# Kernel optimization log

Hardware: AMD Instinct MI355X
Metric: run time of the kernel (lower is better)

Reference implementation:

```python
import jax, jax.numpy as jnp
import numpy as np

N_NODES = 50000
HEADS1 = 4
NEG_SLOPE = 0.2
EPS = 1e-16


def gat_conv(x, edge_index, W, att_src, att_dst, bias, heads, out_ch, concat):
    # edge_index: [2, E] with self-loops already appended by caller
    src, dst = edge_index[0], edge_index[1]
    N = x.shape[0]
    h = (x @ W).reshape(N, heads, out_ch)                      # [N, H, C]
    a_src = jnp.sum(h * att_src, axis=-1)                      # [N, H]
    a_dst = jnp.sum(h * att_dst, axis=-1)                      # [N, H]
    e = a_src[src] + a_dst[dst]                                # [E, H]
    e = jnp.where(e > 0, e, NEG_SLOPE * e)                     # leaky_relu
    m = jax.ops.segment_max(e, dst, num_segments=N)            # [N, H]
    alpha = jnp.exp(e - m[dst])                                # [E, H]
    denom = jax.ops.segment_sum(alpha, dst, num_segments=N)    # [N, H]
    alpha = alpha / (denom[dst] + EPS)                         # [E, H]
    msg = alpha[:, :, None] * h[src]                           # [E, H, C]
    out = jax.ops.segment_sum(msg, dst, num_segments=N)        # [N, H, C]
    if concat:
        out = out.reshape(N, heads * out_ch)
    else:
        out = out.mean(axis=1)
    return out + bias, alpha


def setup_inputs() -> dict:
    key = jax.random.key(0)
    ks = jax.random.split(key, 12)
    N, F, H, heads, C, E = N_NODES, 256, 64, HEADS1, 40, 800000
    g = 0.1
    return {
        "x": jax.random.normal(ks[0], (N, F), dtype=jnp.float32),
        "edge_index": jax.random.randint(ks[1], (2, E), 0, N, dtype=jnp.int32),
        "W1": jax.random.normal(ks[2], (F, heads * H), dtype=jnp.float32) * g,
        "att_src1": jax.random.normal(ks[3], (heads, H), dtype=jnp.float32) * g,
        "att_dst1": jax.random.normal(ks[4], (heads, H), dtype=jnp.float32) * g,
        "b1": jnp.zeros((heads * H,), dtype=jnp.float32),
        "W2": jax.random.normal(ks[5], (heads * H, C), dtype=jnp.float32) * g,
        "att_src2": jax.random.normal(ks[6], (1, C), dtype=jnp.float32) * g,
        "att_dst2": jax.random.normal(ks[7], (1, C), dtype=jnp.float32) * g,
        "b2": jnp.zeros((C,), dtype=jnp.float32),
    }


def reference(x, edge_index, W1, att_src1, att_dst1, b1, W2, att_src2, att_dst2, b2):
    N = x.shape[0]
    # add self-loops (PyG GATConv default)
    loops = jnp.arange(N, dtype=edge_index.dtype)
    ei = jnp.concatenate([edge_index, jnp.stack([loops, loops])], axis=1)
    # dropout is identity in eval mode
    h1, alpha = gat_conv(x, ei, W1, att_src1, att_dst1, b1,
                         HEADS1, W1.shape[1] // HEADS1, concat=True)
    h1 = jax.nn.elu(h1)
    h2, _ = gat_conv(h1, ei, W2, att_src2, att_dst2, b2,
                     1, W2.shape[1], concat=False)
    return jax.nn.log_softmax(h2, axis=1), alpha
```

## Files before the change

kernel.cpp:

```cpp
#include <hip/hip_runtime.h>
#include <math.h>

#define N_NODES 50000
#define HC1 256
#define H1 4
#define C2 40
#define C2P 64
#define E0 800000
#define ET 850000
#define NEG_SLOPE 0.2f
#define EPS_A 1e-16f

typedef __bf16 bf16x8 __attribute__((ext_vector_type(8)));
typedef float f32x4 __attribute__((ext_vector_type(4)));
typedef unsigned short u16x8 __attribute__((ext_vector_type(8)));


__device__ inline unsigned short f2bf(float f) {
    unsigned u = __float_as_uint(f);
    return (unsigned short)((u + 0x7FFFu + ((u >> 16) & 1u)) >> 16);
}
__device__ inline float bf_lo(unsigned q) { return __uint_as_float(q << 16); }
__device__ inline float bf_hi(unsigned q) { return __uint_as_float(q & 0xFFFF0000u); }


__device__ inline int edge_src(const int* __restrict__ ei, int e) {
    return (e < E0) ? ei[e] : (e - E0);
}
__device__ inline int edge_dst(const int* __restrict__ ei, int e) {
    return (e < E0) ? ei[E0 + e] : (e - E0);
}

__device__ inline void acc8(float ac[8], float A, uint4 q) {
    ac[0] += A * bf_lo(q.x); ac[1] += A * bf_hi(q.x);
    ac[2] += A * bf_lo(q.y); ac[3] += A * bf_hi(q.y);
    ac[4] += A * bf_lo(q.z); ac[5] += A * bf_hi(q.z);
    ac[6] += A * bf_lo(q.w); ac[7] += A * bf_hi(q.w);
}

__device__ inline float leaky(float v) { return v > 0.f ? v : NEG_SLOPE * v; }


#define CV_X 3200000
#define CV_W1 65536
#define CV_W2 16384
#define CV_TOT (CV_X + CV_W1 + CV_W2 + N_NODES)

__global__ void convert_all_kernel(const float* __restrict__ x,
                                   const float* __restrict__ W1,
                                   const float* __restrict__ W2,
                                   ushort4* __restrict__ xbf,
                                   unsigned short* __restrict__ w1t,
                                   unsigned short* __restrict__ w2t,
                                   int* __restrict__ deg) {
    int tid = blockIdx.x * blockDim.x + threadIdx.x;
    if (tid < CV_X) {
        float4 v = ((const float4*)x)[tid];
        ushort4 w;
        w.x = f2bf(v.x); w.y = f2bf(v.y); w.z = f2bf(v.z); w.w = f2bf(v.w);
        xbf[tid] = w;
    } else if (tid < CV_X + CV_W1) {
        int i = tid - CV_X;
        int n = i >> 8, k = i & 255;
        w1t[i] = f2bf(W1[k * 256 + n]);
    } else if (tid < CV_X + CV_W1 + CV_W2) {
        int i = tid - CV_X - CV_W1;
        int n = i >> 8, k = i & 255;
        w2t[i] = (n < C2) ? f2bf(W2[k * C2 + n]) : (unsigned short)0;
    } else if (tid < CV_TOT) {
        deg[tid - CV_X - CV_W1 - CV_W2] = 0;
    }
}


__global__ void hist_kernel(const int* __restrict__ ei, int* __restrict__ deg) {
    int e = blockIdx.x * blockDim.x + threadIdx.x;
    if (e >= ET) return;
    atomicAdd(&deg[edge_dst(ei, e)], 1);
}

__global__ __launch_bounds__(256) void scan_block_kernel(const int* __restrict__ deg,
                                                         int* __restrict__ excl,
                                                         int* __restrict__ bsum) {
    __shared__ int tmp[256];
    int t = threadIdx.x;
    int i = blockIdx.x * 256 + t;
    int v = (i < N_NODES) ? deg[i] : 0;
    tmp[t] = v;
    __syncthreads();
#pragma unroll
    for (int o = 1; o < 256; o <<= 1) {
        int x = (t >= o) ? tmp[t - o] : 0;
        __syncthreads();
        tmp[t] += x;
        __syncthreads();
    }
    if (i < N_NODES) excl[i] = tmp[t] - v;
    if (t == 255) bsum[blockIdx.x] = tmp[255];
}

#define NSCAN_B 196

__global__ __launch_bounds__(256) void scan_top_kernel(int* __restrict__ bsum) {
    __shared__ int tmp[256];
    int t = threadIdx.x;
    int v = (t < NSCAN_B) ? bsum[t] : 0;
    tmp[t] = v;
    __syncthreads();
#pragma unroll
    for (int o = 1; o < 256; o <<= 1) {
        int x = (t >= o) ? tmp[t - o] : 0;
        __syncthreads();
        tmp[t] += x;
        __syncthreads();
    }
    if (t < NSCAN_B) bsum[t] = tmp[t] - v;
}

__global__ __launch_bounds__(256) void scan_add_kernel(int* __restrict__ offsets,
                                                       int* __restrict__ cursor,
                                                       const int* __restrict__ bsum) {
    int i = blockIdx.x * 256 + threadIdx.x;
    if (i < N_NODES) {
        int v = offsets[i] + bsum[blockIdx.x];
        offsets[i] = v;
        cursor[i] = v;
    }
    if (i == 0) offsets[N_NODES] = ET;
}

__global__ void scatter_kernel(const int* __restrict__ ei, int* __restrict__ cursor,
                               int2* __restrict__ csr_es) {
    int e = blockIdx.x * blockDim.x + threadIdx.x;
    if (e >= ET) return;
    int d = edge_dst(ei, e);
    int pos = atomicAdd(&cursor[d], 1);
    csr_es[pos] = make_int2(e, edge_src(ei, e));
}


template <int TBM, int TBN, int WROWS, int WCOLS>
__global__ __launch_bounds__(256) void gemm_mfma_kernel(const unsigned short* __restrict__ Abf,
                                                        const unsigned short* __restrict__ Bt,
                                                        unsigned short* __restrict__ Cbf,
                                                        const float* __restrict__ att_s,
                                                        const float* __restrict__ att_d,
                                                        float* __restrict__ a_src_o,
                                                        float* __restrict__ a_dst_o,
                                                        int M, int Nc, int attN, int hstride) {
    static_assert(TBM == WROWS * 64 && TBN == WCOLS * 64, "tile");
    constexpr int LDK = 40;
    __shared__ alignas(16) unsigned short As[TBM * LDK];
    __shared__ alignas(16) unsigned short Bs[TBN * LDK];
    const int t = threadIdx.x;
    const int lane = t & 63;
    const int w = t >> 6;
    const int quad = lane >> 4;
    const int l16 = lane & 15;
    const int wm = (w / WCOLS) * 64;
    const int wn = (w % WCOLS) * 64;
    const int bm = blockIdx.x * TBM;
    const int bn = blockIdx.y * TBN;

    f32x4 acc[4][4] = {};

    for (int k0 = 0; k0 < 256; k0 += 32) {
        __syncthreads();
#pragma unroll
        for (int i = 0; i < TBM / 64; ++i) {
            int idx = t + i * 256;
            int row = idx >> 2, seg = idx & 3;
            u16x8 v = {};
            if (bm + row < M)
                v = *(const u16x8*)(Abf + (size_t)(bm + row) * 256 + k0 + seg * 8);
            *(u16x8*)&As[row * LDK + seg * 8] = v;
        }
#pragma unroll
        for (int i = 0; i < TBN / 64; ++i) {
            int idx = t + i * 256;
            int row = idx >> 2, seg = idx & 3;
            u16x8 v = *(const u16x8*)(Bt + (size_t)(bn + row) * 256 + k0 + seg * 8);
            *(u16x8*)&Bs[row * LDK + seg * 8] = v;
        }
        __syncthreads();

        bf16x8 af[4], bfr[4];
#pragma unroll
        for (int mi = 0; mi < 4; ++mi)
            af[mi] = *(const bf16x8*)&As[(wm + mi * 16 + l16) * LDK + quad * 8];
#pragma unroll
        for (int ni = 0; ni < 4; ++ni)
            bfr[ni] = *(const bf16x8*)&Bs[(wn + ni * 16 + l16) * LDK + quad * 8];
#pragma unroll
        for (int mi = 0; mi < 4; ++mi)
#pragma unroll
            for (int ni = 0; ni < 4; ++ni)
                acc[mi][ni] = __builtin_amdgcn_mfma_f32_16x16x32_bf16(
                    af[mi], bfr[ni], acc[mi][ni], 0, 0, 0);
    }

#pragma unroll
    for (int mi = 0; mi < 4; ++mi)
#pragma unroll
        for (int ni = 0; ni < 4; ++ni)
#pragma unroll
            for (int r = 0; r < 4; ++r) {
                int row = bm + wm + mi * 16 + quad * 4 + r;
                int col = bn + wn + ni * 16 + l16;
                if (row < M)
                    Cbf[(size_t)row * Nc + col] = f2bf(acc[mi][ni][r]);
            }

    float asc[4], adc[4];
#pragma unroll
    for (int ni = 0; ni < 4; ++ni) {
        int col = bn + wn + ni * 16 + l16;
        bool valid = col < attN;
        asc[ni] = valid ? att_s[col] : 0.f;
        adc[ni] = valid ? att_d[col] : 0.f;
    }
    float vs[16], vd[16];
#pragma unroll
    for (int mi = 0; mi < 4; ++mi)
#pragma unroll
        for (int r = 0; r < 4; ++r) {
            float s = 0.f, dd = 0.f;
#pragma unroll
            for (int ni = 0; ni < 4; ++ni) {
                s += acc[mi][ni][r] * asc[ni];
                dd += acc[mi][ni][r] * adc[ni];
            }
            vs[mi * 4 + r] = s;
            vd[mi * 4 + r] = dd;
        }
#pragma unroll
    for (int k = 0; k < 4; ++k) {
        const int o = 1 << k;
        const int b = (l16 >> k) & 1;
#pragma unroll
        for (int j = 0; j < (8 >> k); ++j) {
            float lo = vs[2 * j], hi = vs[2 * j + 1];
            float keep = b ? hi : lo, send = b ? lo : hi;
            vs[j] = keep + __shfl_xor(send, o);
            lo = vd[2 * j]; hi = vd[2 * j + 1];
            keep = b ? hi : lo; send = b ? lo : hi;
            vd[j] = keep + __shfl_xor(send, o);
        }
    }
    {
        int mi = l16 >> 2, r = l16 & 3;
        int row = bm + wm + mi * 16 + quad * 4 + r;
        int head = (bn + wn) >> 6;
        if (row < M) {
            a_src_o[(size_t)row * hstride + head] = vs[0];
            a_dst_o[(size_t)row * hstride + head] = vd[0];
        }
    }
}


#define L1_LOADQ(q, jb)                                                         \
    _Pragma("unroll")                                                           \
    for (int k = 0; k < 4; ++k) {                                               \
        int s_ = __shfl(esy, shbase + (jb) + k);                                \
        q[k] = *(const uint4*)&h1bf[(unsigned)s_ * 128u + 4u * li];             \
    }

#define L1_FMAQ(q, jb)                                                          \
    _Pragma("unroll")                                                           \
    for (int k = 0; k < 4; ++k) {                                               \
        float A_ = aw[4 * ((jb) + k) + headc];                                  \
        acc8(ac, A_, q[k]);                                                     \
    }

__global__ __launch_bounds__(256) void l1_fused_kernel(const int* __restrict__ off,
                                                       const int2* __restrict__ csr_es,
                                                       const float4* __restrict__ a_src4,
                                                       const float4* __restrict__ a_dst4,
                                                       const unsigned* __restrict__ h1bf,
                                                       const float* __restrict__ b1,
                                                       float4* __restrict__ alpha_out4,
                                                       unsigned* __restrict__ out1bf) {
    __shared__ int    s_w[4][2][32];
    __shared__ float4 p_w[4][2][32];
    int t = threadIdx.x;
    int w = t >> 6, lane = t & 63;
    int half = lane >> 5, li = lane & 31;
    int shbase = half << 5;
    int d = blockIdx.x * 8 + w * 2 + half;
    int beg = off[d], end = off[d + 1];
    int deg = end - beg;
    int nch = (deg + 31) >> 5;
    int cnt0 = min(deg, 32);
    bool act0 = li < cnt0;
    float4 ad4 = a_dst4[d];
    int headc = li >> 3;

    float ac[8] = {};
    float4 sum = make_float4(0.f, 0.f, 0.f, 0.f);
    float4 mx = make_float4(-INFINITY, -INFINITY, -INFINITY, -INFINITY);
    int2 es0 = make_int2(0, 0);
    float4 p0 = make_float4(0.f, 0.f, 0.f, 0.f);

    const float* aw = (const float*)&p_w[w][half][0];
    const int*   sw = &s_w[w][half][0];

    if (nch == 1) {
        float4 l0 = make_float4(-INFINITY, -INFINITY, -INFINITY, -INFINITY);
        float4 as4 = make_float4(0.f, 0.f, 0.f, 0.f);
        if (act0) {
            es0 = csr_es[beg + li];
            as4 = a_src4[es0.y];
        }
        int esy = es0.y;
        const int B = (cnt0 + 3) >> 2;

        uint4 qa[4], qb[4];
        L1_LOADQ(qa, 0);
        if (B > 1) { L1_LOADQ(qb, 4); }

        if (act0) {
            l0.x = leaky(as4.x + ad4.x);
            l0.y = leaky(as4.y + ad4.y);
            l0.z = leaky(as4.z + ad4.z);
            l0.w = leaky(as4.w + ad4.w);
        }
        mx = l0;
#pragma unroll
        for (int o = 1; o <= 16; o <<= 1) {
            mx.x = fmaxf(mx.x, __shfl_xor(mx.x, o));
            mx.y = fmaxf(mx.y, __shfl_xor(mx.y, o));
            mx.z = fmaxf(mx.z, __shfl_xor(mx.z, o));
            mx.w = fmaxf(mx.w, __shfl_xor(mx.w, o));
        }
        p0.x = __expf(l0.x - mx.x);
        p0.y = __expf(l0.y - mx.y);
        p0.z = __expf(l0.z - mx.z);
        p0.w = __expf(l0.w - mx.w);
        p_w[w][half][li] = p0;
        sum = p0;

        int i = 0;
        for (; i + 2 <= B; i += 2) {
            L1_FMAQ(qa, i * 4);
            if (i + 2 < B) { L1_LOADQ(qa, (i + 2) * 4); }
            L1_FMAQ(qb, i * 4 + 4);
            if (i + 3 < B) { L1_LOADQ(qb, (i + 3) * 4); }
        }
        if (i < B) { L1_FMAQ(qa, i * 4); }
    } else {
        for (int cc = 0; cc < nch; ++cc) {
            int idx = beg + cc * 32 + li;
            if (idx < end) {
                int2 es = csr_es[idx];
                float4 as4 = a_src4[es.y];
                mx.x = fmaxf(mx.x, leaky(as4.x + ad4.x));
                mx.y = fmaxf(mx.y, leaky(as4.y + ad4.y));
                mx.z = fmaxf(mx.z, leaky(as4.z + ad4.z));
                mx.w = fmaxf(mx.w, leaky(as4.w + ad4.w));
            }
        }
#pragma unroll
        for (int o = 1; o <= 16; o <<= 1) {
            mx.x = fmaxf(mx.x, __shfl_xor(mx.x, o));
            mx.y = fmaxf(mx.y, __shfl_xor(mx.y, o));
            mx.z = fmaxf(mx.z, __shfl_xor(mx.z, o));
            mx.w = fmaxf(mx.w, __shfl_xor(mx.w, o));
        }
        for (int cc = 0; cc < nch; ++cc) {
            int idx = beg + cc * 32 + li;
            if (idx < end) {
                int2 es = csr_es[idx];
                float4 as4 = a_src4[es.y];
                sum.x += __expf(leaky(as4.x + ad4.x) - mx.x);
                sum.y += __expf(leaky(as4.y + ad4.y) - mx.y);
                sum.z += __expf(leaky(as4.z + ad4.z) - mx.z);
                sum.w += __expf(leaky(as4.w + ad4.w) - mx.w);
            }
        }
    }

#pragma unroll
    for (int o = 1; o <= 16; o <<= 1) {
        sum.x += __shfl_xor(sum.x, o);
        sum.y += __shfl_xor(sum.y, o);
        sum.z += __shfl_xor(sum.z, o);
        sum.w += __shfl_xor(sum.w, o);
    }
    float4 inv;
    inv.x = 1.f / (sum.x + EPS_A); inv.y = 1.f / (sum.y + EPS_A);
    inv.z = 1.f / (sum.z + EPS_A); inv.w = 1.f / (sum.w + EPS_A);
    float invh = (headc == 0) ? inv.x : (headc == 1) ? inv.y
               : (headc == 2) ? inv.z : inv.w;

    if (nch == 1) {
        if (act0) {
            float4 al0;
            al0.x = p0.x * inv.x; al0.y = p0.y * inv.y;
            al0.z = p0.z * inv.z; al0.w = p0.w * inv.w;
            alpha_out4[es0.x] = al0;
        }
    } else {
        for (int cc = 0; cc < nch; ++cc) {
            int idx = beg + cc * 32 + li;
            int cnt = min(32, deg - cc * 32);
            if (idx < end) {
                int2 es = csr_es[idx];
                float4 as4 = a_src4[es.y];
                float4 p;
                p.x = __expf(leaky(as4.x + ad4.x) - mx.x);
                p.y = __expf(leaky(as4.y + ad4.y) - mx.y);
                p.z = __expf(leaky(as4.z + ad4.z) - mx.z);
                p.w = __expf(leaky(as4.w + ad4.w) - mx.w);
                float4 al;
                al.x = p.x * inv.x; al.y = p.y * inv.y;
                al.z = p.z * inv.z; al.w = p.w * inv.w;
                alpha_out4[es.x] = al;
                s_w[w][half][li] = es.y;
                p_w[w][half][li] = p;
            }
            for (int j = 0; j < cnt; ++j) {
                int s = sw[j];
                float A = aw[4 * j + headc];
                uint4 q = *(const uint4*)&h1bf[(unsigned)s * 128u + 4u * li];
                acc8(ac, A, q);
            }
        }
    }

#pragma unroll
    for (int c = 0; c < 8; ++c) ac[c] *= invh;

    float4 bb0 = *(const float4*)&b1[8 * li];
    float4 bb1 = *(const float4*)&b1[8 * li + 4];
    float v0 = ac[0] + bb0.x, v1 = ac[1] + bb0.y;
    float v2 = ac[2] + bb0.z, v3 = ac[3] + bb0.w;
    float v4 = ac[4] + bb1.x, v5 = ac[5] + bb1.y;
    float v6 = ac[6] + bb1.z, v7 = ac[7] + bb1.w;
    v0 = v0 > 0.f ? v0 : __expf(v0) - 1.f;
    v1 = v1 > 0.f ? v1 : __expf(v1) - 1.f;
    v2 = v2 > 0.f ? v2 : __expf(v2) - 1.f;
    v3 = v3 > 0.f ? v3 : __expf(v3) - 1.f;
    v4 = v4 > 0.f ? v4 : __expf(v4) - 1.f;
    v5 = v5 > 0.f ? v5 : __expf(v5) - 1.f;
    v6 = v6 > 0.f ? v6 : __expf(v6) - 1.f;
    v7 = v7 > 0.f ? v7 : __expf(v7) - 1.f;
    uint4 qo;
    qo.x = ((unsigned)f2bf(v1) << 16) | (unsigned)f2bf(v0);
    qo.y = ((unsigned)f2bf(v3) << 16) | (unsigned)f2bf(v2);
    qo.z = ((unsigned)f2bf(v5) << 16) | (unsigned)f2bf(v4);
    qo.w = ((unsigned)f2bf(v7) << 16) | (unsigned)f2bf(v6);
    *(uint4*)&out1bf[(size_t)d * 128 + 4 * li] = qo;
}


#define L2_LOADQ(q, jb)                                                         \
    _Pragma("unroll")                                                           \
    for (int k = 0; k < 4; ++k) {                                               \
        int s_ = __shfl(s0, shbase + (jb) + k);                                 \
        q[k] = h2bf[(unsigned)s_ * 32u + li];                                   \
    }

#define L2_FMAQ(q, jb)                                                          \
    _Pragma("unroll")                                                           \
    for (int k = 0; k < 4; ++k) {                                               \
        float A_ = __shfl(p0, shbase + (jb) + k);                               \
        acc0 += A_ * bf_lo(q[k]);                                               \
        acc1 += A_ * bf_hi(q[k]);                                               \
    }

__global__ __launch_bounds__(256) void l2_fused_kernel(const int* __restrict__ off,
                                                       const int2* __restrict__ csr_es,
                                                       const float* __restrict__ a_src,
                                                       const float* __restrict__ a_dst,
                                                       const unsigned* __restrict__ h2bf,
                                                       const float* __restrict__ b2,
                                                       float* __restrict__ out) {
    __shared__ uint2 sp_w[4][2][32];
    int t = threadIdx.x;
    int w = t >> 6, lane = t & 63;
    int half = lane >> 5, li = lane & 31;
    int shbase = half << 5;
    int d = blockIdx.x * 8 + w * 2 + half;
    int beg = off[d], end = off[d + 1];
    int deg = end - beg;
    float ad = a_dst[d];
    int nch = (deg + 31) >> 5;
    int cnt0 = min(deg, 32);
    bool act0 = li < cnt0;

    float sum = 0.f, acc0 = 0.f, acc1 = 0.f;
    float p0 = 0.f;

    if (nch == 1) {
        float el0 = -INFINITY; int s0 = 0;
        if (act0) {
            int2 es = csr_es[beg + li];
            s0 = es.y;
            el0 = leaky(a_src[s0] + ad);
        }
        const int B = (cnt0 + 3) >> 2;
        unsigned qa[4], qb[4];
        L2_LOADQ(qa, 0);
        if (B > 1) { L2_LOADQ(qb, 4); }

        float mx = el0;
#pragma unroll
        for (int o = 1; o <= 16; o <<= 1) mx = fmaxf(mx, __shfl_xor(mx, o));
        p0 = __expf(el0 - mx);
        sum = p0;

        int i = 0;
        for (; i + 2 <= B; i += 2) {
            L2_FMAQ(qa, i * 4);
            if (i + 2 < B) { L2_LOADQ(qa, (i + 2) * 4); }
            L2_FMAQ(qb, i * 4 + 4);
            if (i + 3 < B) { L2_LOADQ(qb, (i + 3) * 4); }
        }
        if (i < B) { L2_FMAQ(qa, i * 4); }
    } else {
        float mx = -INFINITY;
        for (int cc = 0; cc < nch; ++cc) {
            int idx = beg + cc * 32 + li;
            if (idx < end) {
                int2 es = csr_es[idx];
                mx = fmaxf(mx, leaky(a_src[es.y] + ad));
            }
        }
#pragma unroll
        for (int o = 1; o <= 16; o <<= 1) mx = fmaxf(mx, __shfl_xor(mx, o));
        for (int cc = 0; cc < nch; ++cc) {
            int idx = beg + cc * 32 + li;
            int cnt = min(32, deg - cc * 32);
            if (idx < end) {
                int2 es = csr_es[idx];
                float el = leaky(a_src[es.y] + ad);
                float p = __expf(el - mx);
                sum += p;
                sp_w[w][half][li] = make_uint2((unsigned)es.y, __float_as_uint(p));
            }
            for (int j = 0; j < cnt; ++j) {
                uint2 e0 = sp_w[w][half][j];
                float A0 = __uint_as_float(e0.y);
                unsigned q = h2bf[e0.x * 32u + li];
                acc0 += A0 * bf_lo(q);
                acc1 += A0 * bf_hi(q);
            }
        }
    }

#pragma unroll
    for (int o = 1; o <= 16; o <<= 1) sum += __shfl_xor(sum, o);
    float inv = 1.f / (sum + EPS_A);
    acc0 *= inv;
    acc1 *= inv;

    bool act = li < 20;
    float v0 = act ? acc0 + b2[2 * li]     : -INFINITY;
    float v1 = act ? acc1 + b2[2 * li + 1] : -INFINITY;
    float mmx = fmaxf(v0, v1);
#pragma unroll
    for (int o = 16; o; o >>= 1) mmx = fmaxf(mmx, __shfl_xor(mmx, o));
    float ex = act ? __expf(v0 - mmx) + __expf(v1 - mmx) : 0.f;
#pragma unroll
    for (int o = 16; o; o >>= 1) ex += __shfl_xor(ex, o);
    float ls = __logf(ex);
    if (act)
        *(float2*)&out[(size_t)d * C2 + 2 * li] = make_float2(v0 - mmx - ls, v1 - mmx - ls);
}


extern "C" void kernel_launch(void* const* d_in, const int* in_sizes, int n_in,
                              void* d_out, int out_size, void* d_ws, size_t ws_size,
                              hipStream_t stream) {
    const float* x   = (const float*)d_in[0];
    const int*   ei  = (const int*)d_in[1];
    const float* W1  = (const float*)d_in[2];
    const float* as1 = (const float*)d_in[3];
    const float* ad1 = (const float*)d_in[4];
    const float* b1  = (const float*)d_in[5];
    const float* W2  = (const float*)d_in[6];
    const float* as2 = (const float*)d_in[7];
    const float* ad2 = (const float*)d_in[8];
    const float* b2  = (const float*)d_in[9];

    float* out   = (float*)d_out;
    float* alpha = out + (size_t)N_NODES * C2;

    unsigned* u32    = (unsigned*)d_ws;
    unsigned* h1bf   = u32;
    unsigned* xbf    = h1bf + 6400000;
    unsigned* h2bf   = xbf + 6400000;
    unsigned* w1t    = h2bf + 1600000;
    unsigned* w2t    = w1t + 32768;
    float* a_src1    = (float*)(w2t + 8192);
    float* a_dst1    = a_src1 + 200000;
    float* a_src2    = a_dst1 + 200000;
    float* a_dst2    = a_src2 + 50000;
    int*   deg       = (int*)(a_dst2 + 50000);
    int*   offs      = deg + 50000;
    int*   cursor    = offs + 50001;
    int*   bsum      = cursor + 50000;
    int2*  csr_es    = (int2*)(bsum + 257);
    unsigned* out1bf = xbf;

    const int TB = 256;
    const int EB = (ET + TB - 1) / TB;

    convert_all_kernel<<<(CV_TOT + TB - 1) / TB, TB, 0, stream>>>(
        x, W1, W2, (ushort4*)xbf, (unsigned short*)w1t, (unsigned short*)w2t, deg);

    hist_kernel<<<EB, TB, 0, stream>>>(ei, deg);
    scan_block_kernel<<<NSCAN_B, TB, 0, stream>>>(deg, offs, bsum);
    scan_top_kernel<<<1, TB, 0, stream>>>(bsum);
    scan_add_kernel<<<NSCAN_B, TB, 0, stream>>>(offs, cursor, bsum);
    scatter_kernel<<<EB, TB, 0, stream>>>(ei, cursor, csr_es);

    gemm_mfma_kernel<128, 128, 2, 2><<<dim3((N_NODES + 127) / 128, 2), TB, 0, stream>>>(
        (const unsigned short*)xbf, (const unsigned short*)w1t, (unsigned short*)h1bf,
        as1, ad1, a_src1, a_dst1, N_NODES, HC1, 256, H1);
    l1_fused_kernel<<<N_NODES / 8, TB, 0, stream>>>(offs, csr_es,
                                                    (const float4*)a_src1,
                                                    (const float4*)a_dst1,
                                                    h1bf, b1, (float4*)alpha, out1bf);

    gemm_mfma_kernel<256, 64, 4, 1><<<dim3((N_NODES + 255) / 256, 1), TB, 0, stream>>>(
        (const unsigned short*)out1bf, (const unsigned short*)w2t, (unsigned short*)h2bf,
        as2, ad2, a_src2, a_dst2, N_NODES, C2P, C2, 1);
    l2_fused_kernel<<<N_NODES / 8, TB, 0, stream>>>(offs, csr_es, a_src2, a_dst2,
                                                    h2bf, b2, out);
}
```

Baseline: 358.9 us.

## Fuse degree histogram into convert, double-buffer GEMM LDS, batch layer-2 gathers

The degree histogram moves into the conversion kernel, with the deg array zeroed by a memset, which removes one kernel launch. The bf16 GEMM now double-buffers its shared-memory tiles and prefetches the next k-slice before the current MFMAs, dropping one barrier per iteration. The layer-2 single-chunk path issues up to eight gather loads up front instead of a two-deep rotation, which raises memory-level parallelism at the cost of more registers. There is a possible race: the prefetch writes buffer cur^1 after only one barrier, so other waves may still be reading that buffer from the previous iteration.

```diff
diff --git a/kernel.cpp b/kernel.cpp
--- a/kernel.cpp
+++ b/kernel.cpp
@@ -44,11 +44,12 @@
 #define CV_X 3200000
 #define CV_W1 65536
 #define CV_W2 16384
-#define CV_TOT (CV_X + CV_W1 + CV_W2 + N_NODES)
+#define CV_TOT (CV_X + CV_W1 + CV_W2 + ET)
 
 __global__ void convert_all_kernel(const float* __restrict__ x,
                                    const float* __restrict__ W1,
                                    const float* __restrict__ W2,
+                                   const int* __restrict__ ei,
                                    ushort4* __restrict__ xbf,
                                    unsigned short* __restrict__ w1t,
                                    unsigned short* __restrict__ w2t,
@@ -68,16 +69,11 @@
         int n = i >> 8, k = i & 255;
         w2t[i] = (n < C2) ? f2bf(W2[k * C2 + n]) : (unsigned short)0;
     } else if (tid < CV_TOT) {
-        deg[tid - CV_X - CV_W1 - CV_W2] = 0;
-    }
-}
-
-
-__global__ void hist_kernel(const int* __restrict__ ei, int* __restrict__ deg) {
-    int e = blockIdx.x * blockDim.x + threadIdx.x;
-    if (e >= ET) return;
-    atomicAdd(&deg[edge_dst(ei, e)], 1);
-}
+        int e = tid - CV_X - CV_W1 - CV_W2;
+        atomicAdd(&deg[edge_dst(ei, e)], 1);
+    }
+}
+
 
 __global__ __launch_bounds__(256) void scan_block_kernel(const int* __restrict__ deg,
                                                          int* __restrict__ excl,
@@ -138,6 +134,24 @@
     csr_es[pos] = make_int2(e, edge_src(ei, e));
 }
 
+
+#define GEMM_STAGE(k0v, bufv)                                                     \
+    _Pragma("unroll")                                                             \
+    for (int i = 0; i < TBM / 64; ++i) {                                          \
+        int idx = t + i * 256;                                                    \
+        int row = idx >> 2, seg = idx & 3;                                        \
+        u16x8 v = {};                                                             \
+        if (bm + row < M)                                                         \
+            v = *(const u16x8*)(Abf + (size_t)(bm + row) * 256 + (k0v) + seg * 8);\
+        *(u16x8*)&As[bufv][row * LDK + seg * 8] = v;                              \
+    }                                                                             \
+    _Pragma("unroll")                                                             \
+    for (int i = 0; i < TBN / 64; ++i) {                                          \
+        int idx = t + i * 256;                                                    \
+        int row = idx >> 2, seg = idx & 3;                                        \
+        u16x8 v = *(const u16x8*)(Bt + (size_t)(bn + row) * 256 + (k0v) + seg * 8);\
+        *(u16x8*)&Bs[bufv][row * LDK + seg * 8] = v;                              \
+    }
 
 template <int TBM, int TBN, int WROWS, int WCOLS>
 __global__ __launch_bounds__(256) void gemm_mfma_kernel(const unsigned short* __restrict__ Abf,
@@ -150,8 +164,8 @@
                                                         int M, int Nc, int attN, int hstride) {
     static_assert(TBM == WROWS * 64 && TBN == WCOLS * 64, "tile");
     constexpr int LDK = 40;
-    __shared__ alignas(16) unsigned short As[TBM * LDK];
-    __shared__ alignas(16) unsigned short Bs[TBN * LDK];
+    __shared__ alignas(16) unsigned short As[2][TBM * LDK];
+    __shared__ alignas(16) unsigned short Bs[2][TBN * LDK];
     const int t = threadIdx.x;
     const int lane = t & 63;
     const int w = t >> 6;
@@ -164,39 +178,26 @@
 
     f32x4 acc[4][4] = {};
 
+    GEMM_STAGE(0, 0);
+    int cur = 0;
     for (int k0 = 0; k0 < 256; k0 += 32) {
         __syncthreads();
-#pragma unroll
-        for (int i = 0; i < TBM / 64; ++i) {
-            int idx = t + i * 256;
-            int row = idx >> 2, seg = idx & 3;
-            u16x8 v = {};
-            if (bm + row < M)
-                v = *(const u16x8*)(Abf + (size_t)(bm + row) * 256 + k0 + seg * 8);
-            *(u16x8*)&As[row * LDK + seg * 8] = v;
-        }
-#pragma unroll
-        for (int i = 0; i < TBN / 64; ++i) {
-            int idx = t + i * 256;
-            int row = idx >> 2, seg = idx & 3;
-            u16x8 v = *(const u16x8*)(Bt + (size_t)(bn + row) * 256 + k0 + seg * 8);
-            *(u16x8*)&Bs[row * LDK + seg * 8] = v;
-        }
-        __syncthreads();
+        if (k0 + 32 < 256) { GEMM_STAGE(k0 + 32, cur ^ 1); }
 
         bf16x8 af[4], bfr[4];
 #pragma unroll
         for (int mi = 0; mi < 4; ++mi)
-            af[mi] = *(const bf16x8*)&As[(wm + mi * 16 + l16) * LDK + quad * 8];
+            af[mi] = *(const bf16x8*)&As[cur][(wm + mi * 16 + l16) * LDK + quad * 8];
 #pragma unroll
         for (int ni = 0; ni < 4; ++ni)
-            bfr[ni] = *(const bf16x8*)&Bs[(wn + ni * 16 + l16) * LDK + quad * 8];
+            bfr[ni] = *(const bf16x8*)&Bs[cur][(wn + ni * 16 + l16) * LDK + quad * 8];
 #pragma unroll
         for (int mi = 0; mi < 4; ++mi)
 #pragma unroll
             for (int ni = 0; ni < 4; ++ni)
                 acc[mi][ni] = __builtin_amdgcn_mfma_f32_16x16x32_bf16(
                     af[mi], bfr[ni], acc[mi][ni], 0, 0, 0);
+        cur ^= 1;
     }
 
 #pragma unroll
@@ -500,9 +501,10 @@
             el0 = leaky(a_src[s0] + ad);
         }
         const int B = (cnt0 + 3) >> 2;
-        unsigned qa[4], qb[4];
-        L2_LOADQ(qa, 0);
-        if (B > 1) { L2_LOADQ(qb, 4); }
+        unsigned q[8][4];
+#pragma unroll
+        for (int i = 0; i < 8; ++i)
+            if (i < B) { L2_LOADQ(q[i], i * 4); }
 
         float mx = el0;
 #pragma unroll
@@ -510,14 +512,9 @@
         p0 = __expf(el0 - mx);
         sum = p0;
 
-        int i = 0;
-        for (; i + 2 <= B; i += 2) {
-            L2_FMAQ(qa, i * 4);
-            if (i + 2 < B) { L2_LOADQ(qa, (i + 2) * 4); }
-            L2_FMAQ(qb, i * 4 + 4);
-            if (i + 3 < B) { L2_LOADQ(qb, (i + 3) * 4); }
-        }
-        if (i < B) { L2_FMAQ(qa, i * 4); }
+#pragma unroll
+        for (int i = 0; i < 8; ++i)
+            if (i < B) { L2_FMAQ(q[i], i * 4); }
     } else {
         float mx = -INFINITY;
         for (int cc = 0; cc < nch; ++cc) {
@@ -542,9 +539,9 @@
             for (int j = 0; j < cnt; ++j) {
                 uint2 e0 = sp_w[w][half][j];
                 float A0 = __uint_as_float(e0.y);
-                unsigned q = h2bf[e0.x * 32u + li];
-                acc0 += A0 * bf_lo(q);
-                acc1 += A0 * bf_hi(q);
+                unsigned qv = h2bf[e0.x * 32u + li];
+                acc0 += A0 * bf_lo(qv);
+                acc1 += A0 * bf_hi(qv);
             }
         }
     }
@@ -607,10 +604,11 @@
     const int TB = 256;
     const int EB = (ET + TB - 1) / TB;
 
+    hipMemsetAsync(deg, 0, (size_t)N_NODES * sizeof(int), stream);
+
     convert_all_kernel<<<(CV_TOT + TB - 1) / TB, TB, 0, stream>>>(
-        x, W1, W2, (ushort4*)xbf, (unsigned short*)w1t, (unsigned short*)w2t, deg);
-
-    hist_kernel<<<EB, TB, 0, stream>>>(ei, deg);
+        x, W1, W2, ei, (ushort4*)xbf, (unsigned short*)w1t, (unsigned short*)w2t, deg);
+
     scan_block_kernel<<<NSCAN_B, TB, 0, stream>>>(deg, offs, bsum);
     scan_top_kernel<<<1, TB, 0, stream>>>(bsum);
     scan_add_kernel<<<NSCAN_B, TB, 0, stream>>>(offs, cursor, bsum);
```

After: 356.4 us. No clear change (-0.7%).
